# Optimization experiments

Hardware: AMD Instinct MI355X
Metric: run time of the kernel (lower is better)

## Reference

```python
import jax, jax.numpy as jnp
import numpy as np

WIN = 25            # window size (win_h == win_w == 25)
DIM = 256           # channels
DIM_HEAD = 32
HEADS = DIM // DIM_HEAD   # 8
HIDDEN = int(DIM * 2.0)   # mlp_ratio = 2.0
EPS = 1e-5


def _rel_pos_indices(w=WIN):
    # replicates the buffer built in Attention.__init__
    pos = np.arange(w)
    gi, gj = np.meshgrid(pos, pos, indexing='ij')
    grid = np.stack([gi.ravel(), gj.ravel()], axis=-1)          # (w*w, 2)
    rel = grid[:, None, :] - grid[None, :, :] + (w - 1)          # (n, n, 2)
    return jnp.asarray(rel[..., 0] * (2 * w - 1) + rel[..., 1])  # (n, n) int


def setup_inputs() -> dict:
    key = jax.random.key(0)
    ks = jax.random.split(key, 8)
    s = 0.02
    d = DIM
    return {
        'x': jax.random.normal(ks[0], (2, d, 100, 100), jnp.float32),
        'w_qkv': jax.random.normal(ks[1], (3 * d, d), jnp.float32) * s,
        'w_out': jax.random.normal(ks[2], (d, d), jnp.float32) * s,
        'rel_bias_table': jax.random.normal(ks[3], ((2 * WIN - 1) ** 2, HEADS), jnp.float32) * s,
        'gamma2': jnp.ones((d,), jnp.float32),
        'beta2': jnp.zeros((d,), jnp.float32),
        'w1': jax.random.normal(ks[4], (HIDDEN, d), jnp.float32) * s,
        'b1': jnp.zeros((HIDDEN,), jnp.float32),
        'w2': jax.random.normal(ks[5], (d, HIDDEN), jnp.float32) * s,
        'b2': jnp.zeros((d,), jnp.float32),
    }


def _layernorm(x, g, b, eps=EPS):
    m = x.mean(-1, keepdims=True)
    v = ((x - m) ** 2).mean(-1, keepdims=True)
    return (x - m) / jnp.sqrt(v + eps) * g + b


def reference(x, w_qkv, w_out, rel_bias_table, gamma2, beta2, w1, b1, w2, b2):
    b, d, H, W = x.shape
    nh, nw = H // WIN, W // WIN
    h, dh = HEADS, DIM_HEAD
    scale = dh ** -0.5
    n = WIN * WIN

    # --- window partition: (b, d, H, W) -> (b*nh*nw, n, d) ---
    xw = x.reshape(b, d, nh, WIN, nw, WIN).transpose(0, 2, 4, 3, 5, 1)
    xw = xw.reshape(b * nh * nw, n, d)

    # --- windowed attention with relative-position bias (norm1 unused in source) ---
    qkv = xw @ w_qkv.T                         # (B, n, 3d)
    q, k, v = jnp.split(qkv, 3, axis=-1)
    split_heads = lambda t: t.reshape(t.shape[0], n, h, dh).transpose(0, 2, 1, 3)
    q = split_heads(q) * scale                 # (B, h, n, dh)
    k = split_heads(k)
    v = split_heads(v)

    sim = jnp.einsum('bhid,bhjd->bhij', q, k)  # (B, h, n, n)
    bias = rel_bias_table[_rel_pos_indices()]  # (n, n, h)
    sim = sim + bias.transpose(2, 0, 1)[None]
    attn = jax.nn.softmax(sim, axis=-1)
    out = jnp.einsum('bhij,bhjd->bhid', attn, v)            # (B, h, n, dh)
    out = out.transpose(0, 2, 1, 3).reshape(-1, n, d)        # head-major concat: (m d)
    out = out @ w_out.T                                      # (B, n, d)

    # --- un-partition: (b*nh*nw, n, d) -> (b, d, H, W) ---
    xa = out.reshape(b, nh, nw, WIN, WIN, d).transpose(0, 5, 1, 3, 2, 4)
    xa = xa.reshape(b, d, H, W)

    # --- norm2 + MLP + residual ---
    y = xa.transpose(0, 2, 3, 1).reshape(b, H * W, d)
    y = _layernorm(y, gamma2, beta2)
    y = jax.nn.gelu(y @ w1.T + b1, approximate=False) @ w2.T + b2
    y = y.reshape(b, H, W, d).transpose(0, 3, 1, 2)
    return x + y
```

## Files before the change

kernel.cpp:

```cpp
#include <hip/hip_runtime.h>


using f32x4 = __attribute__((ext_vector_type(4))) float;
using s16x8 = __attribute__((ext_vector_type(8))) short;
using u32x4 = __attribute__((ext_vector_type(4))) unsigned;

__device__ __forceinline__ ushort f2b(float f) {
  union { float f; unsigned u; } v; v.f = f;
  return (ushort)((v.u + 0x7FFFu + ((v.u >> 16) & 1u)) >> 16);
}
__device__ __forceinline__ ushort f2b_fast(float f) {
  union { float f; unsigned u; } v; v.f = f;
  return (ushort)((v.u + 0x8000u) >> 16);
}
__device__ __forceinline__ float b2f(ushort u) {
  union { unsigned u; float f; } v; v.u = ((unsigned)u) << 16; return v.f;
}
__device__ __forceinline__ float lo2f(unsigned w) {
  union { unsigned u; float f; } v; v.u = w << 16; return v.f;
}
__device__ __forceinline__ float hi2f(unsigned w) {
  union { unsigned u; float f; } v; v.u = w & 0xffff0000u; return v.f;
}

__device__ __forceinline__ unsigned cvtpk(float lo, float hi) {
  unsigned r;
  asm("v_cvt_pk_bf16_f32 %0, %1, %2" : "=v"(r) : "v"(lo), "v"(hi));
  return r;
}
__device__ __forceinline__ void pl32(unsigned& a, unsigned& b) {
  asm("v_permlane32_swap_b32 %0, %1" : "+v"(a), "+v"(b));
}
__device__ __forceinline__ void pl16(unsigned& a, unsigned& b) {
  asm("v_permlane16_swap_b32 %0, %1" : "+v"(a), "+v"(b));
}

__device__ __forceinline__ void gld16(const void* g, void* l) {
  __builtin_amdgcn_global_load_lds((const __attribute__((address_space(1))) void*)g,
                                   (__attribute__((address_space(3))) void*)l, 16, 0, 0);
}

template<int KB>
__device__ __forceinline__ void gemm_core(const ushort* __restrict__ A, int lda,
                                          const ushort* __restrict__ B, int ldb,
                                          f32x4 acc[4][4]) {
  __shared__ ushort As[128 * 64];
  __shared__ ushort Bs[128 * 64];
  const int tid = threadIdx.x;
  const int lane = tid & 63;
  const int wv = tid >> 6;
  const int wr = (wv >> 1) * 64;
  const int wc = (wv & 1) * 64;
  const int srow = (lane >> 3);
  const int sg = ((lane & 7) ^ (srow & 7)) * 8;
  f32x4 zero = {0.f, 0.f, 0.f, 0.f};
#pragma unroll
  for (int mt = 0; mt < 4; ++mt)
#pragma unroll
    for (int nt = 0; nt < 4; ++nt) acc[mt][nt] = zero;

  for (int kb = 0; kb < KB; ++kb) {
#pragma unroll
    for (int j = 0; j < 4; ++j) {
      int r0 = wv * 32 + j * 8;
      int row = r0 + srow;
      gld16(A + row * lda + kb * 64 + sg, &As[r0 * 64]);
      gld16(B + row * ldb + kb * 64 + sg, &Bs[r0 * 64]);
    }
    __syncthreads();
#pragma unroll
    for (int ks = 0; ks < 2; ++ks) {
      s16x8 af[4], bfr[4];
      const int G = ks * 4 + (lane >> 4);
#pragma unroll
      for (int mt = 0; mt < 4; ++mt) {
        int row = wr + mt * 16 + (lane & 15);
        af[mt] = *(const s16x8*)&As[row * 64 + (G ^ (row & 7)) * 8];
      }
#pragma unroll
      for (int nt = 0; nt < 4; ++nt) {
        int row = wc + nt * 16 + (lane & 15);
        bfr[nt] = *(const s16x8*)&Bs[row * 64 + (G ^ (row & 7)) * 8];
      }
#pragma unroll
      for (int mt = 0; mt < 4; ++mt)
#pragma unroll
        for (int nt = 0; nt < 4; ++nt)
          acc[mt][nt] = __builtin_amdgcn_mfma_f32_16x16x32_bf16(af[mt], bfr[nt], acc[mt][nt], 0, 0, 0);
    }
    __syncthreads();
  }
}

__global__ __launch_bounds__(256) void k_prep(const float* __restrict__ x,
                                              const float* __restrict__ wqkv,
                                              const float* __restrict__ wout,
                                              const float* __restrict__ w1,
                                              const float* __restrict__ w2,
                                              const float* __restrict__ table,
                                              ushort* __restrict__ Xw,
                                              ushort* __restrict__ wqkvb,
                                              ushort* __restrict__ woutb,
                                              ushort* __restrict__ w1b,
                                              ushort* __restrict__ w2b,
                                              ushort* __restrict__ biasPh) {
  __shared__ ushort smem[64 * 264];
  const int bid = blockIdx.x, tid = threadIdx.x;
  if (bid < 320) {
    ushort (*Ls)[264] = (ushort(*)[264])smem;
    const int t0 = bid * 64;
    const int w = t0 / 640;
    const int tokbase = t0 - w * 640;
    const int b = w >> 4, wh = (w >> 2) & 3, ww = w & 3;
    for (int i = tid; i < 64 * 256; i += 256) {
      int c = i >> 6, tl = i & 63;
      int tok = tokbase + tl;
      ushort val = 0;
      if (tok < 625) {
        int ii = tok / 25, jj = tok - ii * 25;
        val = f2b(x[((b * 256 + c) * 100 + wh * 25 + ii) * 100 + ww * 25 + jj]);
      }
      Ls[tl][c] = val;
    }
    __syncthreads();
    for (int i = tid; i < 64 * 32; i += 256) {
      int tl = i >> 5, g = (i & 31) * 8;
      *(uint4*)(Xw + (t0 + tl) * 256 + g) = *(const uint4*)&Ls[tl][g];
    }
  } else if (bid < 832) {
    int v = (bid - 320) * 1024 + tid * 4;
    const float* src; ushort* dst; int off;
    if (v < 196608)      { src = wqkv; dst = wqkvb; off = v; }
    else if (v < 262144) { src = wout; dst = woutb; off = v - 196608; }
    else if (v < 393216) { src = w1;   dst = w1b;   off = v - 262144; }
    else                 { src = w2;   dst = w2b;   off = v - 393216; }
    float4 f = *(const float4*)(src + off);
    ushort4 u; u.x = f2b(f.x); u.y = f2b(f.y); u.z = f2b(f.z); u.w = f2b(f.w);
    *(ushort4*)(dst + off) = u;
  } else {
    float* tl = (float*)smem;
    const int qb = bid - 832;
    const int h = qb / 40, t = qb - (qb / 40) * 40;
    for (int i = tid; i < 2401; i += 256) tl[i] = table[i * 8 + h] * 1.4426950408889634f;
    __syncthreads();
    const int lane = tid >> 2, rr = tid & 3;
    const int quad = lane >> 4, cl = lane & 15;
    int qrow = t * 16 + cl;
    int qg = (qrow < 625) ? qrow : 0;
    const int ri = qg / 25, ci = qg - ri * 25;
    for (int cc = 0; cc < 4; ++cc)
      for (int cp = 0; cp < 5; ++cp)
#pragma unroll
        for (int codd = 0; codd < 2; ++codd) {
          int kv = cc * 160 + (cp * 2 + codd) * 16 + quad * 4 + rr;
          float v = -1e30f;
          if (kv < 625) {
            int rj = kv / 25, cj = kv - rj * 25;
            v = tl[(ri - rj + 24) * 49 + (ci - cj + 24)];
          }
          biasPh[((((h * 40 + t) * 4 + cc) * 5 + cp) * 64 + lane) * 8 + codd * 4 + rr] = f2b(v);
        }
  }
}

__global__ __launch_bounds__(256) void k_qkv(const ushort* __restrict__ Xw,
                                             const ushort* __restrict__ Wb,
                                             ushort* __restrict__ Qb,
                                             ushort* __restrict__ Kb,
                                             ushort* __restrict__ VbT) {
  f32x4 acc[4][4];
  gemm_core<4>(Xw + blockIdx.x * 128 * 256, 256, Wb + blockIdx.y * 128 * 256, 256, acc);
  const int lane = threadIdx.x & 63, wv = threadIdx.x >> 6;
  const int wr = (wv >> 1) * 64, wc = (wv & 1) * 64;
  const int which = blockIdx.y >> 1;
  const float QSC = 0.17677669529663687f * 1.4426950408889634f;
#pragma unroll
  for (int mt = 0; mt < 4; ++mt) {
#pragma unroll
    for (int nt = 0; nt < 4; ++nt) {
      int n = blockIdx.y * 128 + wc + nt * 16 + (lane & 15);
      int h = (n >> 5) & 7, ch = n & 31;
      int m0 = blockIdx.x * 128 + wr + mt * 16 + (lane >> 4) * 4;
      int w = m0 / 640, tok0 = m0 - w * 640;
      if (which == 2) {
        ushort4 pk;
        pk.x = f2b_fast(acc[mt][nt][0]); pk.y = f2b_fast(acc[mt][nt][1]);
        pk.z = f2b_fast(acc[mt][nt][2]); pk.w = f2b_fast(acc[mt][nt][3]);
        *(ushort4*)(VbT + (((w << 3) + h) * 32 + ch) * 640 + tok0) = pk;
      } else {
        ushort* dst = which == 0 ? Qb : Kb;
        float sc = which == 0 ? QSC : 1.f;
#pragma unroll
        for (int r = 0; r < 4; ++r)
          dst[(((w << 3) + h) * 640 + tok0 + r) * 32 + ch] = f2b_fast(acc[mt][nt][r] * sc);
      }
    }
  }
}

__global__ __launch_bounds__(256, 3) void k_attn(const ushort* __restrict__ Qb,
                                                 const ushort* __restrict__ Kb,
                                                 const ushort* __restrict__ VbT,
                                                 const ushort* __restrict__ biasPh,
                                                 ushort* __restrict__ AO) {
  const int tid = threadIdx.x;
  const int lane = tid & 63;
  const int wv = tid >> 6;
  const int quad = lane >> 4;
  const int cl = lane & 15;
  const int bid = blockIdx.x;
  const int h = bid & 7;
  const int rem = bid >> 3;
  const int win = rem / 5;
  const int tg = rem - win * 5;
  const ushort* Qg = Qb + (win * 8 + h) * 20480;
  const ushort* Kg = Kb + (win * 8 + h) * 20480;
  const ushort* Vt = VbT + (win * 8 + h) * 20480;

  const int t0 = tg * 8 + wv * 2;
  const s16x8 qf0 = *(const s16x8*)(Qg + (t0 * 16 + cl) * 32 + quad * 8);
  const s16x8 qf1 = *(const s16x8*)(Qg + ((t0 + 1) * 16 + cl) * 32 + quad * 8);
  s16x8 ones;
#pragma unroll
  for (int j = 0; j < 8; ++j) ones[j] = (short)0x3F80;

  const f32x4 zero = {0.f, 0.f, 0.f, 0.f};
  f32x4 o00 = zero, o01 = zero, o10 = zero, o11 = zero;
  f32x4 sum0 = zero, sum1 = zero;

#pragma unroll
  for (int cc = 0; cc < 4; ++cc) {
    s16x8 kf[10];
#pragma unroll
    for (int c = 0; c < 10; ++c)
      kf[c] = *(const s16x8*)(Kg + (cc * 160 + c * 16 + cl) * 32 + quad * 8);
    s16x8 vf0[5], vf1[5];
#pragma unroll
    for (int kc = 0; kc < 5; ++kc) {
      vf0[kc] = *(const s16x8*)(Vt + cl * 640 + cc * 160 + kc * 32 + quad * 8);
      vf1[kc] = *(const s16x8*)(Vt + (16 + cl) * 640 + cc * 160 + kc * 32 + quad * 8);
    }
#pragma unroll
    for (int tlp = 0; tlp < 2; ++tlp) {
      const int t = t0 + tlp;
      const s16x8 qf = tlp ? qf1 : qf0;
      const ushort* bp = biasPh + (((h * 40 + t) * 4 + cc) * 5) * 512 + lane * 8;
      f32x4 s[10];
#pragma unroll
      for (int cp = 0; cp < 5; ++cp) {
        s16x8 bb = *(const s16x8*)(bp + cp * 512);
        const unsigned* bw = (const unsigned*)&bb;
        f32x4 c0, c1;
        c0[0] = lo2f(bw[0]); c0[1] = hi2f(bw[0]); c0[2] = lo2f(bw[1]); c0[3] = hi2f(bw[1]);
        c1[0] = lo2f(bw[2]); c1[1] = hi2f(bw[2]); c1[2] = lo2f(bw[3]); c1[3] = hi2f(bw[3]);
        s[cp * 2] = c0; s[cp * 2 + 1] = c1;
      }
#pragma unroll
      for (int c = 0; c < 10; ++c)
        s[c] = __builtin_amdgcn_mfma_f32_16x16x32_bf16(kf[c], qf, s[c], 0, 0, 0);
#pragma unroll
      for (int c = 0; c < 10; ++c)
#pragma unroll
        for (int r = 0; r < 4; ++r) s[c][r] = exp2f(s[c][r]);
      f32x4& o0 = tlp ? o10 : o00;
      f32x4& o1 = tlp ? o11 : o01;
      f32x4& sm = tlp ? sum1 : sum0;
#pragma unroll
      for (int kc = 0; kc < 5; ++kc) {
        unsigned a0 = cvtpk(s[2 * kc][0], s[2 * kc][1]);
        unsigned a1 = cvtpk(s[2 * kc][2], s[2 * kc][3]);
        unsigned b0 = cvtpk(s[2 * kc + 1][0], s[2 * kc + 1][1]);
        unsigned b1 = cvtpk(s[2 * kc + 1][2], s[2 * kc + 1][3]);
        pl32(a0, b0); pl16(a0, b0);
        pl32(a1, b1); pl16(a1, b1);
        u32x4 pw; pw[0] = a0; pw[1] = a1; pw[2] = b0; pw[3] = b1;
        s16x8 pf = __builtin_bit_cast(s16x8, pw);
        o0 = __builtin_amdgcn_mfma_f32_16x16x32_bf16(vf0[kc], pf, o0, 0, 0, 0);
        o1 = __builtin_amdgcn_mfma_f32_16x16x32_bf16(vf1[kc], pf, o1, 0, 0, 0);
        sm = __builtin_amdgcn_mfma_f32_16x16x32_bf16(ones, pf, sm, 0, 0, 0);
      }
    }
  }
#pragma unroll
  for (int tlp = 0; tlp < 2; ++tlp) {
    const f32x4& o0 = tlp ? o10 : o00;
    const f32x4& o1 = tlp ? o11 : o01;
    const f32x4& sm = tlp ? sum1 : sum0;
    int tok = (t0 + tlp) * 16 + cl;
    if (tok < 625) {
      float inv = 1.f / sm[0];
      int base = (win * 640 + tok) * 256 + h * 32 + quad * 4;
      ushort4 p0, p1;
      p0.x = f2b_fast(o0[0] * inv); p0.y = f2b_fast(o0[1] * inv);
      p0.z = f2b_fast(o0[2] * inv); p0.w = f2b_fast(o0[3] * inv);
      p1.x = f2b_fast(o1[0] * inv); p1.y = f2b_fast(o1[1] * inv);
      p1.z = f2b_fast(o1[2] * inv); p1.w = f2b_fast(o1[3] * inv);
      *(ushort4*)(AO + base) = p0;
      *(ushort4*)(AO + base + 16) = p1;
    }
  }
}

__global__ __launch_bounds__(256, 2) void k_out_ln(const ushort* __restrict__ AO,
                                                   const ushort* __restrict__ Wb,
                                                   const float* __restrict__ gamma,
                                                   const float* __restrict__ beta,
                                                   ushort* __restrict__ Yn) {
  __shared__ ushort As[64 * 64];
  __shared__ ushort Bs[256 * 64];
  __shared__ float red[2][64][2];
  const int tid = threadIdx.x;
  const int lane = tid & 63;
  const int wv = tid >> 6;
  const int wr = (wv >> 1) * 32, wc = (wv & 1) * 128;
  const int quad = lane >> 4, cl = lane & 15;
  const int srow = lane >> 3;
  const int sg = ((lane & 7) ^ (srow & 7)) * 8;
  f32x4 zero = {0.f, 0.f, 0.f, 0.f};
  f32x4 acc[2][8];
#pragma unroll
  for (int mt = 0; mt < 2; ++mt)
#pragma unroll
    for (int nt = 0; nt < 8; ++nt) acc[mt][nt] = zero;

  const ushort* A = AO + blockIdx.x * 64 * 256;
  for (int kb = 0; kb < 4; ++kb) {
#pragma unroll
    for (int i = 0; i < 10; ++i) {
      int r0 = (wv + i * 4) * 8;
      int row = r0 + srow;
      if (r0 < 64) gld16(A + row * 256 + kb * 64 + sg, &As[r0 * 64]);
      else         gld16(Wb + (row - 64) * 256 + kb * 64 + sg, &Bs[(r0 - 64) * 64]);
    }
    __syncthreads();
#pragma unroll
    for (int ks = 0; ks < 2; ++ks) {
      s16x8 af[2], bfr[8];
      const int G = ks * 4 + quad;
#pragma unroll
      for (int mt = 0; mt < 2; ++mt) {
        int row = wr + mt * 16 + cl;
        af[mt] = *(const s16x8*)&As[row * 64 + (G ^ (row & 7)) * 8];
      }
#pragma unroll
      for (int nt = 0; nt < 8; ++nt) {
        int row = wc + nt * 16 + cl;
        bfr[nt] = *(const s16x8*)&Bs[row * 64 + (G ^ (row & 7)) * 8];
      }
#pragma unroll
      for (int mt = 0; mt < 2; ++mt)
#pragma unroll
        for (int nt = 0; nt < 8; ++nt)
          acc[mt][nt] = __builtin_amdgcn_mfma_f32_16x16x32_bf16(af[mt], bfr[nt], acc[mt][nt], 0, 0, 0);
    }
    __syncthreads();
  }
#pragma unroll
  for (int mt = 0; mt < 2; ++mt)
#pragma unroll
    for (int r = 0; r < 4; ++r) {
      float s = 0.f, ss = 0.f;
#pragma unroll
      for (int nt = 0; nt < 8; ++nt) { float v = acc[mt][nt][r]; s += v; ss += v * v; }
      s += __shfl_xor(s, 1, 64); ss += __shfl_xor(ss, 1, 64);
      s += __shfl_xor(s, 2, 64); ss += __shfl_xor(ss, 2, 64);
      s += __shfl_xor(s, 4, 64); ss += __shfl_xor(ss, 4, 64);
      s += __shfl_xor(s, 8, 64); ss += __shfl_xor(ss, 8, 64);
      if (cl == 0) {
        int row = wr + mt * 16 + quad * 4 + r;
        red[wc >> 7][row][0] = s;
        red[wc >> 7][row][1] = ss;
      }
    }
  __syncthreads();
  float g[8], bt[8];
#pragma unroll
  for (int nt = 0; nt < 8; ++nt) { int n = wc + nt * 16 + cl; g[nt] = gamma[n]; bt[nt] = beta[n]; }
  const int m0 = blockIdx.x * 64;
#pragma unroll
  for (int mt = 0; mt < 2; ++mt)
#pragma unroll
    for (int r = 0; r < 4; ++r) {
      int row = wr + mt * 16 + quad * 4 + r;
      int m = m0 + row;
      int w = m / 640, tok = m - w * 640;
      if (tok < 625) {
        float sum = red[0][row][0] + red[1][row][0];
        float ssum = red[0][row][1] + red[1][row][1];
        float mean = sum * 0.00390625f;
        float var = ssum * 0.00390625f - mean * mean;
        float rstd = rsqrtf(var + 1e-5f);
        int b = w >> 4, whh = (w >> 2) & 3, www = w & 3;
        int ii = tok / 25, jj = tok - ii * 25;
        int p = (whh * 25 + ii) * 100 + www * 25 + jj;
        ushort* dst = Yn + (b * 10000 + p) * 256;
#pragma unroll
        for (int nt = 0; nt < 8; ++nt) {
          float v = (acc[mt][nt][r] - mean) * rstd * g[nt] + bt[nt];
          dst[wc + nt * 16 + cl] = f2b_fast(v);
        }
      }
    }
}

__global__ __launch_bounds__(256) void k_fc1(const ushort* __restrict__ Yn,
                                             const ushort* __restrict__ W1b,
                                             const float* __restrict__ b1,
                                             ushort* __restrict__ G) {
  f32x4 acc[4][4];
  gemm_core<4>(Yn + blockIdx.x * 128 * 256, 256, W1b + blockIdx.y * 128 * 256, 256, acc);
  const int lane = threadIdx.x & 63, wv = threadIdx.x >> 6;
  const int wr = (wv >> 1) * 64, wc = (wv & 1) * 64;
#pragma unroll
  for (int mt = 0; mt < 4; ++mt)
#pragma unroll
    for (int nt = 0; nt < 4; ++nt) {
      int n = blockIdx.y * 128 + wc + nt * 16 + (lane & 15);
      float bias = b1[n];
#pragma unroll
      for (int r = 0; r < 4; ++r) {
        int m = blockIdx.x * 128 + wr + mt * 16 + (lane >> 4) * 4 + r;
        float v = acc[mt][nt][r] + bias;
        v = 0.5f * v * (1.f + erff(v * 0.70710678118f));
        G[m * 512 + n] = f2b_fast(v);
      }
    }
}

__global__ __launch_bounds__(256) void k_fc2(const ushort* __restrict__ W2b,
                                             const ushort* __restrict__ G,
                                             const float* __restrict__ b2,
                                             const float* __restrict__ x,
                                             float* __restrict__ out) {
  f32x4 acc[4][4];
  gemm_core<8>(W2b + blockIdx.x * 128 * 512, 512, G + blockIdx.y * 128 * 512, 512, acc);
  const int lane = threadIdx.x & 63, wv = threadIdx.x >> 6;
  const int wr = (wv >> 1) * 64, wc = (wv & 1) * 64;
#pragma unroll
  for (int mt = 0; mt < 4; ++mt)
#pragma unroll
    for (int nt = 0; nt < 4; ++nt) {
      int t = blockIdx.y * 128 + wc + nt * 16 + (lane & 15);
      if (t < 20000) {
        int b = t / 10000, p = t - b * 10000;
#pragma unroll
        for (int r = 0; r < 4; ++r) {
          int c = blockIdx.x * 128 + wr + mt * 16 + (lane >> 4) * 4 + r;
          int idx = (b * 256 + c) * 10000 + p;
          out[idx] = x[idx] + acc[mt][nt][r] + b2[c];
        }
      }
    }
}

extern "C" void kernel_launch(void* const* d_in, const int* in_sizes, int n_in,
                              void* d_out, int out_size, void* d_ws, size_t ws_size,
                              hipStream_t stream) {
  const float* x     = (const float*)d_in[0];
  const float* wqkv  = (const float*)d_in[1];
  const float* wout  = (const float*)d_in[2];
  const float* bias  = (const float*)d_in[3];
  const float* gamma = (const float*)d_in[4];
  const float* beta  = (const float*)d_in[5];
  const float* w1    = (const float*)d_in[6];
  const float* b1    = (const float*)d_in[7];
  const float* w2    = (const float*)d_in[8];
  const float* b2    = (const float*)d_in[9];
  float* out = (float*)d_out;
  char* ws = (char*)d_ws;

  ushort* Xw    = (ushort*)(ws + 0);
  ushort* AO    = Xw;
  ushort* wqkvb = (ushort*)(ws + 10485760);
  ushort* woutb = (ushort*)(ws + 10878976);
  ushort* w1b   = (ushort*)(ws + 11010048);
  ushort* w2b   = (ushort*)(ws + 11272192);
  ushort* Qb    = (ushort*)(ws + 11534336);
  ushort* Kb    = (ushort*)(ws + 22020096);
  ushort* VbT   = (ushort*)(ws + 32505856);
  ushort* biasPh= (ushort*)(ws + 42991616);
  ushort* Yn    = (ushort*)(ws + 22020096);
  ushort* G     = (ushort*)(ws + 32505856);

  k_prep  <<<1152, 256, 0, stream>>>(x, wqkv, wout, w1, w2, bias,
                                     Xw, wqkvb, woutb, w1b, w2b, biasPh);
  k_qkv   <<<dim3(160, 6), 256, 0, stream>>>(Xw, wqkvb, Qb, Kb, VbT);
  k_attn  <<<1280, 256, 0, stream>>>(Qb, Kb, VbT, biasPh, AO);
  k_out_ln<<<320, 256, 0, stream>>>(AO, woutb, gamma, beta, Yn);
  k_fc1   <<<dim3(157, 4), 256, 0, stream>>>(Yn, w1b, b1, G);
  k_fc2   <<<dim3(2, 157), 256, 0, stream>>>(w2b, G, b2, x, out);
}
```

Measured before the change: 225.9 us.

## Restructure attention inner loop into per-32-key chunks to cut register pressure

The attention kernel's inner loop now loads the K, V and bias fragments for one 32-key chunk at a time and interleaves the QK, exp2 and PV MFMAs per chunk, instead of preloading 10 K fragments and holding 10 score tiles. This shrinks the live register set so launch bounds can be raised from 3 to 4 blocks per SIMD for more occupancy. exp2f is also swapped for the raw hardware exp2 intrinsic. The risk is less instruction-level parallelism and latency hiding per wave, plus exp2 precision or denormal differences.

```diff
diff --git a/kernel.cpp b/kernel.cpp
--- a/kernel.cpp
+++ b/kernel.cpp
@@ -198,7 +198,7 @@
   }
 }
 
-__global__ __launch_bounds__(256, 3) void k_attn(const ushort* __restrict__ Qb,
+__global__ __launch_bounds__(256, 4) void k_attn(const ushort* __restrict__ Qb,
                                                  const ushort* __restrict__ Kb,
                                                  const ushort* __restrict__ VbT,
                                                  const ushort* __restrict__ biasPh,
@@ -228,55 +228,44 @@
   f32x4 o00 = zero, o01 = zero, o10 = zero, o11 = zero;
   f32x4 sum0 = zero, sum1 = zero;
 
+  const ushort* bp0 = biasPh + ((h * 40 + t0) * 20) * 512 + lane * 8;
+
 #pragma unroll
   for (int cc = 0; cc < 4; ++cc) {
-    s16x8 kf[10];
-#pragma unroll
-    for (int c = 0; c < 10; ++c)
-      kf[c] = *(const s16x8*)(Kg + (cc * 160 + c * 16 + cl) * 32 + quad * 8);
-    s16x8 vf0[5], vf1[5];
 #pragma unroll
     for (int kc = 0; kc < 5; ++kc) {
-      vf0[kc] = *(const s16x8*)(Vt + cl * 640 + cc * 160 + kc * 32 + quad * 8);
-      vf1[kc] = *(const s16x8*)(Vt + (16 + cl) * 640 + cc * 160 + kc * 32 + quad * 8);
-    }
-#pragma unroll
-    for (int tlp = 0; tlp < 2; ++tlp) {
-      const int t = t0 + tlp;
-      const s16x8 qf = tlp ? qf1 : qf0;
-      const ushort* bp = biasPh + (((h * 40 + t) * 4 + cc) * 5) * 512 + lane * 8;
-      f32x4 s[10];
-#pragma unroll
-      for (int cp = 0; cp < 5; ++cp) {
-        s16x8 bb = *(const s16x8*)(bp + cp * 512);
+      const s16x8 kfA = *(const s16x8*)(Kg + (cc * 160 + (2 * kc) * 16 + cl) * 32 + quad * 8);
+      const s16x8 kfB = *(const s16x8*)(Kg + (cc * 160 + (2 * kc + 1) * 16 + cl) * 32 + quad * 8);
+      const s16x8 vfa = *(const s16x8*)(Vt + cl * 640 + cc * 160 + kc * 32 + quad * 8);
+      const s16x8 vfb = *(const s16x8*)(Vt + (16 + cl) * 640 + cc * 160 + kc * 32 + quad * 8);
+#pragma unroll
+      for (int tlp = 0; tlp < 2; ++tlp) {
+        const s16x8 qf = tlp ? qf1 : qf0;
+        s16x8 bb = *(const s16x8*)(bp0 + (tlp * 20 + cc * 5 + kc) * 512);
         const unsigned* bw = (const unsigned*)&bb;
         f32x4 c0, c1;
         c0[0] = lo2f(bw[0]); c0[1] = hi2f(bw[0]); c0[2] = lo2f(bw[1]); c0[3] = hi2f(bw[1]);
         c1[0] = lo2f(bw[2]); c1[1] = hi2f(bw[2]); c1[2] = lo2f(bw[3]); c1[3] = hi2f(bw[3]);
-        s[cp * 2] = c0; s[cp * 2 + 1] = c1;
-      }
-#pragma unroll
-      for (int c = 0; c < 10; ++c)
-        s[c] = __builtin_amdgcn_mfma_f32_16x16x32_bf16(kf[c], qf, s[c], 0, 0, 0);
-#pragma unroll
-      for (int c = 0; c < 10; ++c)
-#pragma unroll
-        for (int r = 0; r < 4; ++r) s[c][r] = exp2f(s[c][r]);
-      f32x4& o0 = tlp ? o10 : o00;
-      f32x4& o1 = tlp ? o11 : o01;
-      f32x4& sm = tlp ? sum1 : sum0;
-#pragma unroll
-      for (int kc = 0; kc < 5; ++kc) {
-        unsigned a0 = cvtpk(s[2 * kc][0], s[2 * kc][1]);
-        unsigned a1 = cvtpk(s[2 * kc][2], s[2 * kc][3]);
-        unsigned b0 = cvtpk(s[2 * kc + 1][0], s[2 * kc + 1][1]);
-        unsigned b1 = cvtpk(s[2 * kc + 1][2], s[2 * kc + 1][3]);
+        f32x4 s0 = __builtin_amdgcn_mfma_f32_16x16x32_bf16(kfA, qf, c0, 0, 0, 0);
+        f32x4 s1 = __builtin_amdgcn_mfma_f32_16x16x32_bf16(kfB, qf, c1, 0, 0, 0);
+#pragma unroll
+        for (int r = 0; r < 4; ++r) {
+          s0[r] = __builtin_amdgcn_exp2f(s0[r]);
+          s1[r] = __builtin_amdgcn_exp2f(s1[r]);
+        }
+        unsigned a0 = cvtpk(s0[0], s0[1]);
+        unsigned a1 = cvtpk(s0[2], s0[3]);
+        unsigned b0 = cvtpk(s1[0], s1[1]);
+        unsigned b1 = cvtpk(s1[2], s1[3]);
         pl32(a0, b0); pl16(a0, b0);
         pl32(a1, b1); pl16(a1, b1);
         u32x4 pw; pw[0] = a0; pw[1] = a1; pw[2] = b0; pw[3] = b1;
         s16x8 pf = __builtin_bit_cast(s16x8, pw);
-        o0 = __builtin_amdgcn_mfma_f32_16x16x32_bf16(vf0[kc], pf, o0, 0, 0, 0);
-        o1 = __builtin_amdgcn_mfma_f32_16x16x32_bf16(vf1[kc], pf, o1, 0, 0, 0);
+        f32x4& o0 = tlp ? o10 : o00;
+        f32x4& o1 = tlp ? o11 : o01;
+        f32x4& sm = tlp ? sum1 : sum0;
+        o0 = __builtin_amdgcn_mfma_f32_16x16x32_bf16(vfa, pf, o0, 0, 0, 0);
+        o1 = __builtin_amdgcn_mfma_f32_16x16x32_bf16(vfb, pf, o1, 0, 0, 0);
         sm = __builtin_amdgcn_mfma_f32_16x16x32_bf16(ones, pf, sm, 0, 0, 0);
       }
     }
```

Measured after the change: 223.5 us. Within noise of the previous version (-1.0%).
